# Kernel tuning notes

Hardware: AMD Instinct MI355X
Metric: run time of the kernel (lower is better)

## Reference

```python
import jax, jax.numpy as jnp
import numpy as np

P = 5  # patchsize == stride (non-overlapping)


def unfold_patches(x, p):
    # x: [N, C, H, W] -> [N, L, C, p, p], blocks ordered row-major (matches F.unfold)
    N, C, H, W = x.shape
    x = x.reshape(N, C, H // p, p, W // p, p)
    return x.transpose(0, 2, 4, 1, 3, 5).reshape(N, (H // p) * (W // p), C, p, p)


def fold_patches(pat, H, W, p):
    # [N, L, C, p, p] -> [N, C, H, W]; stride==kernel so F.fold is pure placement (no overlap sums)
    N, L, C, _, _ = pat.shape
    x = pat.reshape(N, H // p, W // p, C, p, p)
    return x.transpose(0, 3, 1, 4, 2, 5).reshape(N, C, H, W)


def gather_scale_concat(fold, idx, gamma):
    # fold: [N, L, C, p, p]; idx: [N, L, 4] int; gamma: [4]
    def gath(k):
        return jnp.take_along_axis(fold, idx[:, :, k][:, :, None, None, None], axis=1)
    # first slot uses patch j itself (not idx[...,0]), per the original loop body
    return jnp.concatenate(
        [gamma[0] * fold, gamma[1] * gath(1), gamma[2] * gath(2), gamma[3] * gath(3)], axis=2)


def conv3x3(x, w, b):
    y = jax.lax.conv_general_dilated(x, w, window_strides=(1, 1), padding='SAME',
                                     dimension_numbers=('NCHW', 'OIHW', 'NCHW'))
    return y + b[None, :, None, None]


def setup_inputs() -> dict:
    key = jax.random.key(0)
    ks = jax.random.split(key, 7)
    N, C, H, W = 4, 32, 300, 300
    L = (H // P) * (W // P)
    x_rgb = jax.random.normal(ks[0], (N, C, H, W), dtype=jnp.float32)
    y_hsi = jax.random.normal(ks[1], (N, C, H, W), dtype=jnp.float32)
    corr = jax.random.randint(ks[2], (2, N, L, 4), 0, L)
    rgb_gamma = jnp.ones((4,), jnp.float32)
    hsi_gamma = jnp.ones((4,), jnp.float32)
    rgb_W = jax.random.normal(ks[3], (C, 4 * C, 3, 3), dtype=jnp.float32) * 0.02
    rgb_b = jnp.zeros((C,), jnp.float32)
    hsi_W = jax.random.normal(ks[4], (C, 4 * C, 3, 3), dtype=jnp.float32) * 0.02
    hsi_b = jnp.zeros((C,), jnp.float32)
    return {'x_rgb': x_rgb, 'y_hsi': y_hsi, 'corr': corr,
            'rgb_gamma': rgb_gamma, 'hsi_gamma': hsi_gamma,
            'rgb_W': rgb_W, 'rgb_b': rgb_b, 'hsi_W': hsi_W, 'hsi_b': hsi_b}


def reference(x_rgb, y_hsi, corr, rgb_gamma, hsi_gamma, rgb_W, rgb_b, hsi_W, hsi_b):
    n_feats = x_rgb.shape[1]
    half = n_feats // 2
    H, W = x_rgb.shape[2], x_rgb.shape[3]
    hsi = jnp.concatenate([x_rgb[:, :half], y_hsi[:, :half]], axis=1)      # [N, n_feats, H, W]
    rgb = jnp.concatenate([x_rgb[:, half:n_feats], y_hsi[:, half:n_feats]], axis=1)
    idx = corr[0]  # [N, L, 4]
    # H, W divisible by P -> calc_padding yields zero padding
    fold_rgb = unfold_patches(rgb, P)  # [N, L, C, p, p]
    fold_hsi = unfold_patches(hsi, P)
    patch_rgb = gather_scale_concat(fold_rgb, idx, rgb_gamma)  # [N, L, 4C, p, p]
    patch_hsi = gather_scale_concat(fold_hsi, idx, hsi_gamma)
    img_rgb = fold_patches(patch_rgb, H, W, P)  # [N, 4C, H, W]
    img_hsi = fold_patches(patch_hsi, H, W, P)
    out_rgb = conv3x3(img_rgb, rgb_W, rgb_b) + rgb
    out_hsi = conv3x3(img_hsi, hsi_W, hsi_b) + hsi
    return (out_rgb, out_hsi)
```

## Files before the change

### kernel.cpp

```cpp
#include <hip/hip_runtime.h>

#define HW        90000
#define OUT_HALF  11520000
#define CPLANE    11520000ull
#define WPACK_OFF  46080000ull
#define WS_NEED    (46080000ull + 147456ull)

typedef short short8 __attribute__((ext_vector_type(8)));
typedef float f32x4  __attribute__((ext_vector_type(4)));

__device__ inline short f2bf(float f) {
    unsigned u = __builtin_bit_cast(unsigned, f);
    u += 0x7fff + ((u >> 16) & 1);
    return (short)(u >> 16);
}
__device__ inline float bf2f(short s) {
    unsigned u = ((unsigned)(unsigned short)s) << 16;
    return __builtin_bit_cast(float, u);
}

__global__ __launch_bounds__(256)
void pack_weights(const float* __restrict__ wR, const float* __restrict__ wH,
                  const float* __restrict__ rg, const float* __restrict__ hg,
                  short* __restrict__ wpack) {
    int id = blockIdx.x * 256 + threadIdx.x;
    if (id >= 73728) return;
    int e    = id & 7;
    int lane = (id >> 3) & 63;
    int h    = (id >> 9) & 1;
    int t    = (id >> 10) % 9;
    int kb   = ((id >> 10) / 9) & 3;
    int conv = id / 36864;
    int co   = h * 16 + (lane & 15);
    int cin  = kb * 32 + (lane >> 4) * 8 + e;
    const float* w = conv ? wH : wR;
    const float* g = conv ? hg : rg;
    wpack[id] = f2bf(w[(co * 128 + cin) * 9 + t] * g[cin >> 5]);
}

__global__ __launch_bounds__(256)
void nchw2nhwc(const float* __restrict__ xrgb, const float* __restrict__ yhsi,
               short* __restrict__ cmb) {
    int wave = threadIdx.x >> 6, lane = threadIdx.x & 63;
    if (lane >= 60) return;
    int y = blockIdx.y * 4 + wave;
    int x = blockIdx.x * 60 + lane;
    int n = blockIdx.z;
    const float* xb = xrgb + n * 32 * HW + y * 300 + x;
    const float* yb = yhsi + n * 32 * HW + y * 300 + x;
    size_t pxo = ((size_t)n * HW + y * 300 + x) * 32;
    short* d0 = cmb + pxo;
    short* d1 = cmb + CPLANE + pxo;
    #pragma unroll
    for (int q = 0; q < 4; ++q) {
        short8 v0, v1;
        #pragma unroll
        for (int e = 0; e < 8; ++e) {
            int c = q * 8 + e;
            v0[e] = f2bf((c < 16) ? xb[(16 + c) * HW] : yb[c * HW]);
            v1[e] = f2bf((c < 16) ? xb[c * HW] : yb[(c - 16) * HW]);
        }
        *(short8*)(d0 + q * 8) = v0;
        *(short8*)(d1 + q * 8) = v1;
    }
}

__global__ __launch_bounds__(256, 5)
void conv_mfma(const short* __restrict__ cmb_all, const short* __restrict__ wpack,
               const int* __restrict__ corr,
               const float* __restrict__ bR, const float* __restrict__ bH,
               float* __restrict__ out) {
    __shared__ alignas(16) char lds[2][16128];
    int tile = blockIdx.x;
    int n = blockIdx.y;
    int conv = blockIdx.z;
    int ty = tile / 19, tx = tile - ty * 19;
    int y0 = ty * 12, x0 = tx * 16;
    int tid = threadIdx.x;

    const short* cmb = cmb_all + conv * CPLANE + (size_t)n * HW * 32;
    const short* wp  = wpack + conv * 36864;

    bool stager = tid < 252;
    int sj = 0, sintra = 0;
    const int* scr = corr;
    bool svalid = false;
    if (stager) {
        int hr = tid / 18, hc = tid - hr * 18;
        int gy = y0 + hr - 1, gx = x0 + hc - 1;
        svalid = (gy >= 0 && gy < 300 && gx >= 0 && gx < 300);
        if (svalid) {
            int pr = gy / 5, pc = gx / 5;
            sj = pr * 60 + pc;
            sintra = (gy - pr * 5) * 300 + (gx - pc * 5);
            scr = corr + (n * 3600 + sj) * 4;
        }
    }
    int swz = (tid & 7) << 4;

    #define STAGE(buf, k)                                                        \
        do {                                                                     \
            short8 v0 = {0,0,0,0,0,0,0,0}, v1 = v0, v2 = v0, v3 = v0;            \
            if (svalid) {                                                        \
                int jp = ((k) == 0) ? sj : scr[(k)];                             \
                int soff = (jp / 60) * 1500 + (jp % 60) * 5 + sintra;            \
                const short8* s = (const short8*)(cmb + (size_t)soff * 32);      \
                v0 = s[0]; v1 = s[1]; v2 = s[2]; v3 = s[3];                      \
            }                                                                    \
            char* d = lds[(buf)];                                                \
            int b0 = tid * 64;                                                   \
            *(short8*)(d + ((b0 +  0) ^ swz)) = v0;                              \
            *(short8*)(d + ((b0 + 16) ^ swz)) = v1;                              \
            *(short8*)(d + ((b0 + 32) ^ swz)) = v2;                              \
            *(short8*)(d + ((b0 + 48) ^ swz)) = v3;                              \
        } while (0)

    if (stager) STAGE(0, 0);
    __syncthreads();

    int wave = tid >> 6, lane = tid & 63;
    int l15 = lane & 15, lh = lane >> 4;

    f32x4 acc[3][2];
    #pragma unroll
    for (int g = 0; g < 3; ++g)
        #pragma unroll
        for (int h = 0; h < 2; ++h)
            acc[g][h] = (f32x4){0.f, 0.f, 0.f, 0.f};

    #pragma unroll
    for (int kb = 0; kb < 4; ++kb) {
        if (kb < 3 && stager) STAGE((kb + 1) & 1, kb + 1);
        const char* base = lds[kb & 1];
        #pragma unroll
        for (int t = 0; t < 9; ++t) {
            int dy = t / 3 - 1, dx = t % 3 - 1;
            short8 a0 = *(const short8*)(wp + (((kb * 9 + t) * 2 + 0) * 64 + lane) * 8);
            short8 a1 = *(const short8*)(wp + (((kb * 9 + t) * 2 + 1) * 64 + lane) * 8);
            #pragma unroll
            for (int g = 0; g < 3; ++g) {
                int hp = (wave * 3 + g + dy + 1) * 18 + (l15 + dx + 1);
                short8 b = *(const short8*)(base + ((hp * 64 + lh * 16) ^ ((hp & 7) << 4)));
                acc[g][0] = __builtin_amdgcn_mfma_f32_16x16x32_bf16(a0, b, acc[g][0], 0, 0, 0);
                acc[g][1] = __builtin_amdgcn_mfma_f32_16x16x32_bf16(a1, b, acc[g][1], 0, 0, 0);
            }
        }
        __syncthreads();
    }

    const float* bias = conv ? bH : bR;
    #pragma unroll
    for (int g = 0; g < 3; ++g) {
        int gy = y0 + wave * 3 + g;
        int gx = x0 + l15;
        if (gx < 300) {
            int pixo = gy * 300 + gx;
            const short* resp = cmb + (size_t)pixo * 32;
            short8 r0 = *(const short8*)(resp);
            short8 r1 = *(const short8*)(resp + 8);
            short8 r2 = *(const short8*)(resp + 16);
            short8 r3 = *(const short8*)(resp + 24);
            #pragma unroll
            for (int h = 0; h < 2; ++h) {
                #pragma unroll
                for (int reg = 0; reg < 4; ++reg) {
                    int co = h * 16 + lh * 4 + reg;
                    int q = co >> 3, e = co & 7;
                    float res = bf2f(q == 0 ? r0[e] : q == 1 ? r1[e] : q == 2 ? r2[e] : r3[e]);
                    out[conv * OUT_HALF + (n * 32 + co) * HW + pixo] = acc[g][h][reg] + bias[co] + res;
                }
            }
        }
    }
    #undef STAGE
}

__global__ __launch_bounds__(256)
void fused_gather_conv(const float* __restrict__ xrgb, const float* __restrict__ yhsi,
                       const int* __restrict__ corr, const float* __restrict__ rgb_gamma,
                       const float* __restrict__ hsi_gamma, const float* __restrict__ wR,
                       const float* __restrict__ bR, const float* __restrict__ wH,
                       const float* __restrict__ bH, float* __restrict__ out) {
    int tid = blockIdx.x * blockDim.x + threadIdx.x;
    if (tid >= 4 * HW) return;
    int n = tid / HW, pix = tid - n * HW;
    int y = pix / 300, x = pix - y * 300;
    const int* idx = corr + n * (3600 * 4);
    const float* xb = xrgb + n * (32 * HW);
    const float* yb = yhsi + n * (32 * HW);
    float accR[32], accH[32];
    #pragma unroll
    for (int i = 0; i < 32; ++i) { accR[i] = 0.f; accH[i] = 0.f; }
    for (int k = 0; k < 4; ++k) {
        float gr = rgb_gamma[k], gh = hsi_gamma[k];
        int off[9];
        #pragma unroll
        for (int t = 0; t < 9; ++t) {
            int dy = t / 3 - 1, dx = t % 3 - 1;
            int yy = y + dy, xx = x + dx;
            int o = -1;
            if (yy >= 0 && yy < 300 && xx >= 0 && xx < 300) {
                int pr = yy / 5, pc = xx / 5;
                int j = pr * 60 + pc;
                int jp = (k == 0) ? j : idx[j * 4 + k];
                o = ((jp / 60) * 5 + (yy - pr * 5)) * 300 + (jp % 60) * 5 + (xx - pc * 5);
            }
            off[t] = o;
        }
        for (int c = 0; c < 32; ++c) {
            const float* srcR = (c < 16) ? (xb + (16 + c) * HW) : (yb + c * HW);
            const float* srcH = (c < 16) ? (xb + c * HW) : (yb + (c - 16) * HW);
            float vr[9], vh[9];
            #pragma unroll
            for (int t = 0; t < 9; ++t) {
                bool vld = off[t] >= 0;
                vr[t] = vld ? gr * srcR[off[t]] : 0.f;
                vh[t] = vld ? gh * srcH[off[t]] : 0.f;
            }
            const float* wRp = wR + (k * 32 + c) * 9;
            const float* wHp = wH + (k * 32 + c) * 9;
            #pragma unroll
            for (int t = 0; t < 9; ++t)
                #pragma unroll
                for (int co = 0; co < 32; ++co) {
                    accR[co] = fmaf(vr[t], wRp[co * 1152 + t], accR[co]);
                    accH[co] = fmaf(vh[t], wHp[co * 1152 + t], accH[co]);
                }
        }
    }
    #pragma unroll
    for (int co = 0; co < 32; ++co) {
        float resR = (co < 16) ? xb[(16 + co) * HW + pix] : yb[co * HW + pix];
        float resH = (co < 16) ? xb[co * HW + pix] : yb[(co - 16) * HW + pix];
        out[(n * 32 + co) * HW + pix]            = accR[co] + bR[co] + resR;
        out[OUT_HALF + (n * 32 + co) * HW + pix] = accH[co] + bH[co] + resH;
    }
}

extern "C" void kernel_launch(void* const* d_in, const int* in_sizes, int n_in,
                              void* d_out, int out_size, void* d_ws, size_t ws_size,
                              hipStream_t stream) {
    const float* xrgb = (const float*)d_in[0];
    const float* yhsi = (const float*)d_in[1];
    const int*   corr = (const int*)d_in[2];
    const float* rg   = (const float*)d_in[3];
    const float* hg   = (const float*)d_in[4];
    const float* wR   = (const float*)d_in[5];
    const float* bR   = (const float*)d_in[6];
    const float* wH   = (const float*)d_in[7];
    const float* bH   = (const float*)d_in[8];
    float* out = (float*)d_out;

    if (ws_size >= WS_NEED) {
        short* cmb   = (short*)d_ws;
        short* wpack = (short*)((char*)d_ws + WPACK_OFF);
        hipLaunchKernelGGL(pack_weights, dim3(288), dim3(256), 0, stream, wR, wH, rg, hg, wpack);
        hipLaunchKernelGGL(nchw2nhwc, dim3(5, 75, 4), dim3(256), 0, stream, xrgb, yhsi, cmb);
        hipLaunchKernelGGL(conv_mfma, dim3(475, 4, 2), dim3(256), 0, stream,
                           cmb, wpack, corr, bR, bH, out);
    } else {
        int total = 4 * HW;
        hipLaunchKernelGGL(fused_gather_conv, dim3((total + 255) / 256), dim3(256), 0, stream,
                           xrgb, yhsi, corr, rg, hg, wR, bR, wH, bH, out);
    }
}
```

Measured before the change: 148.0 us.

## Enlarge conv tile to 16x16 with register reuse of halo rows

Each block now covers a 16x16 output tile instead of 12x16, with each wave computing four rows. The halo grows to 18x18, staged two pixels per thread. The inner loop is reordered by dx: it loads the three weight fragments and six LDS rows once, then reuses them across the 4x3 row/dy combinations. This cuts LDS reads and halo overhead per output, and the corr lookups and source offsets are precomputed once. In exchange it uses more registers and LDS, so occupancy is lowered to 3 blocks, and bottom tiles waste some work.

```diff
diff --git a/kernel.cpp b/kernel.cpp
--- a/kernel.cpp
+++ b/kernel.cpp
@@ -65,95 +65,132 @@
     }
 }
 
-__global__ __launch_bounds__(256, 5)
+__global__ __launch_bounds__(256, 3)
 void conv_mfma(const short* __restrict__ cmb_all, const short* __restrict__ wpack,
                const int* __restrict__ corr,
                const float* __restrict__ bR, const float* __restrict__ bH,
                float* __restrict__ out) {
-    __shared__ alignas(16) char lds[2][16128];
+    __shared__ alignas(16) char lds[2][20736];
     int tile = blockIdx.x;
     int n = blockIdx.y;
     int conv = blockIdx.z;
     int ty = tile / 19, tx = tile - ty * 19;
-    int y0 = ty * 12, x0 = tx * 16;
+    int y0 = ty * 16, x0 = tx * 16;
     int tid = threadIdx.x;
 
     const short* cmb = cmb_all + conv * CPLANE + (size_t)n * HW * 32;
     const short* wp  = wpack + conv * 36864;
 
-    bool stager = tid < 252;
-    int sj = 0, sintra = 0;
-    const int* scr = corr;
-    bool svalid = false;
-    if (stager) {
-        int hr = tid / 18, hc = tid - hr * 18;
+    int  pA = tid, pB = tid + 256;
+    bool hasB = pB < 324;
+    bool vA = false, vB = false;
+    int sA0=0,sA1=0,sA2=0,sA3=0, sB0=0,sB1=0,sB2=0,sB3=0;
+    {
+        int hr = pA / 18, hc = pA - hr * 18;
         int gy = y0 + hr - 1, gx = x0 + hc - 1;
-        svalid = (gy >= 0 && gy < 300 && gx >= 0 && gx < 300);
-        if (svalid) {
+        vA = (gy >= 0 && gy < 300 && gx >= 0 && gx < 300);
+        if (vA) {
             int pr = gy / 5, pc = gx / 5;
-            sj = pr * 60 + pc;
-            sintra = (gy - pr * 5) * 300 + (gx - pc * 5);
-            scr = corr + (n * 3600 + sj) * 4;
-        }
-    }
-    int swz = (tid & 7) << 4;
-
-    #define STAGE(buf, k)                                                        \
+            int sj = pr * 60 + pc;
+            int sintra = (gy - pr * 5) * 300 + (gx - pc * 5);
+            const int* scr = corr + (n * 3600 + sj) * 4;
+            int j1 = scr[1], j2 = scr[2], j3 = scr[3];
+            sA0 = (sj / 60) * 1500 + (sj % 60) * 5 + sintra;
+            sA1 = (j1 / 60) * 1500 + (j1 % 60) * 5 + sintra;
+            sA2 = (j2 / 60) * 1500 + (j2 % 60) * 5 + sintra;
+            sA3 = (j3 / 60) * 1500 + (j3 % 60) * 5 + sintra;
+        }
+    }
+    if (hasB) {
+        int hr = pB / 18, hc = pB - hr * 18;
+        int gy = y0 + hr - 1, gx = x0 + hc - 1;
+        vB = (gy >= 0 && gy < 300 && gx >= 0 && gx < 300);
+        if (vB) {
+            int pr = gy / 5, pc = gx / 5;
+            int sj = pr * 60 + pc;
+            int sintra = (gy - pr * 5) * 300 + (gx - pc * 5);
+            const int* scr = corr + (n * 3600 + sj) * 4;
+            int j1 = scr[1], j2 = scr[2], j3 = scr[3];
+            sB0 = (sj / 60) * 1500 + (sj % 60) * 5 + sintra;
+            sB1 = (j1 / 60) * 1500 + (j1 % 60) * 5 + sintra;
+            sB2 = (j2 / 60) * 1500 + (j2 % 60) * 5 + sintra;
+            sB3 = (j3 / 60) * 1500 + (j3 % 60) * 5 + sintra;
+        }
+    }
+
+    #define STAGE1(buf, px, valid, soff)                                         \
         do {                                                                     \
             short8 v0 = {0,0,0,0,0,0,0,0}, v1 = v0, v2 = v0, v3 = v0;            \
-            if (svalid) {                                                        \
-                int jp = ((k) == 0) ? sj : scr[(k)];                             \
-                int soff = (jp / 60) * 1500 + (jp % 60) * 5 + sintra;            \
-                const short8* s = (const short8*)(cmb + (size_t)soff * 32);      \
+            if (valid) {                                                         \
+                const short8* s = (const short8*)(cmb + (size_t)(soff) * 32);    \
                 v0 = s[0]; v1 = s[1]; v2 = s[2]; v3 = s[3];                      \
             }                                                                    \
             char* d = lds[(buf)];                                                \
-            int b0 = tid * 64;                                                   \
-            *(short8*)(d + ((b0 +  0) ^ swz)) = v0;                              \
-            *(short8*)(d + ((b0 + 16) ^ swz)) = v1;                              \
-            *(short8*)(d + ((b0 + 32) ^ swz)) = v2;                              \
-            *(short8*)(d + ((b0 + 48) ^ swz)) = v3;                              \
+            int b0 = (px) * 64, sz = ((px) & 7) << 4;                            \
+            *(short8*)(d + ((b0 +  0) ^ sz)) = v0;                               \
+            *(short8*)(d + ((b0 + 16) ^ sz)) = v1;                               \
+            *(short8*)(d + ((b0 + 32) ^ sz)) = v2;                               \
+            *(short8*)(d + ((b0 + 48) ^ sz)) = v3;                               \
         } while (0)
-
-    if (stager) STAGE(0, 0);
+    #define STAGE(buf, k)                                                        \
+        do {                                                                     \
+            STAGE1(buf, pA, vA, sA##k);                                          \
+            if (hasB) STAGE1(buf, pB, vB, sB##k);                                \
+        } while (0)
+
+    STAGE(0, 0);
     __syncthreads();
 
     int wave = tid >> 6, lane = tid & 63;
     int l15 = lane & 15, lh = lane >> 4;
-
-    f32x4 acc[3][2];
-    #pragma unroll
-    for (int g = 0; g < 3; ++g)
+    int wr = wave * 4;
+
+    f32x4 acc[4][2];
+    #pragma unroll
+    for (int g = 0; g < 4; ++g)
         #pragma unroll
         for (int h = 0; h < 2; ++h)
             acc[g][h] = (f32x4){0.f, 0.f, 0.f, 0.f};
 
     #pragma unroll
     for (int kb = 0; kb < 4; ++kb) {
-        if (kb < 3 && stager) STAGE((kb + 1) & 1, kb + 1);
+        if (kb == 0) STAGE(1, 1);
+        if (kb == 1) STAGE(0, 2);
+        if (kb == 2) STAGE(1, 3);
         const char* base = lds[kb & 1];
         #pragma unroll
-        for (int t = 0; t < 9; ++t) {
-            int dy = t / 3 - 1, dx = t % 3 - 1;
-            short8 a0 = *(const short8*)(wp + (((kb * 9 + t) * 2 + 0) * 64 + lane) * 8);
-            short8 a1 = *(const short8*)(wp + (((kb * 9 + t) * 2 + 1) * 64 + lane) * 8);
-            #pragma unroll
-            for (int g = 0; g < 3; ++g) {
-                int hp = (wave * 3 + g + dy + 1) * 18 + (l15 + dx + 1);
-                short8 b = *(const short8*)(base + ((hp * 64 + lh * 16) ^ ((hp & 7) << 4)));
-                acc[g][0] = __builtin_amdgcn_mfma_f32_16x16x32_bf16(a0, b, acc[g][0], 0, 0, 0);
-                acc[g][1] = __builtin_amdgcn_mfma_f32_16x16x32_bf16(a1, b, acc[g][1], 0, 0, 0);
-            }
-        }
-        __syncthreads();
+        for (int dxi = 0; dxi < 3; ++dxi) {
+            short8 a[3][2];
+            #pragma unroll
+            for (int dyi = 0; dyi < 3; ++dyi) {
+                int t = dyi * 3 + dxi;
+                a[dyi][0] = *(const short8*)(wp + (((kb * 9 + t) * 2 + 0) * 64 + lane) * 8);
+                a[dyi][1] = *(const short8*)(wp + (((kb * 9 + t) * 2 + 1) * 64 + lane) * 8);
+            }
+            short8 b[6];
+            #pragma unroll
+            for (int rr = 0; rr < 6; ++rr) {
+                int hp = (wr + rr) * 18 + (l15 + dxi);
+                b[rr] = *(const short8*)(base + ((hp * 64 + lh * 16) ^ ((hp & 7) << 4)));
+            }
+            #pragma unroll
+            for (int g = 0; g < 4; ++g) {
+                #pragma unroll
+                for (int dyi = 0; dyi < 3; ++dyi) {
+                    acc[g][0] = __builtin_amdgcn_mfma_f32_16x16x32_bf16(a[dyi][0], b[g + dyi], acc[g][0], 0, 0, 0);
+                    acc[g][1] = __builtin_amdgcn_mfma_f32_16x16x32_bf16(a[dyi][1], b[g + dyi], acc[g][1], 0, 0, 0);
+                }
+            }
+        }
+        if (kb < 3) __syncthreads();
     }
 
     const float* bias = conv ? bH : bR;
     #pragma unroll
-    for (int g = 0; g < 3; ++g) {
-        int gy = y0 + wave * 3 + g;
+    for (int g = 0; g < 4; ++g) {
+        int gy = y0 + wr + g;
         int gx = x0 + l15;
-        if (gx < 300) {
+        if (gy < 300 && gx < 300) {
             int pixo = gy * 300 + gx;
             const short* resp = cmb + (size_t)pixo * 32;
             short8 r0 = *(const short8*)(resp);
@@ -173,6 +210,7 @@
         }
     }
     #undef STAGE
+    #undef STAGE1
 }
 
 __global__ __launch_bounds__(256)
@@ -256,7 +294,7 @@
         short* wpack = (short*)((char*)d_ws + WPACK_OFF);
         hipLaunchKernelGGL(pack_weights, dim3(288), dim3(256), 0, stream, wR, wH, rg, hg, wpack);
         hipLaunchKernelGGL(nchw2nhwc, dim3(5, 75, 4), dim3(256), 0, stream, xrgb, yhsi, cmb);
-        hipLaunchKernelGGL(conv_mfma, dim3(475, 4, 2), dim3(256), 0, stream,
+        hipLaunchKernelGGL(conv_mfma, dim3(361, 4, 2), dim3(256), 0, stream,
                            cmb, wpack, corr, bR, bH, out);
     } else {
         int total = 4 * HW;
```

After: 137.8 us. 1.07x faster.
